# Kernel tuning notes

Hardware: AMD Instinct MI355X
Metric: run time of the kernel (lower is better)

The kernel has to match this reference:

```python
import jax, jax.numpy as jnp
from jax import lax
import numpy as np

K = 2        # k-hop MIS / number of rw SpGEMM iterations
EPS = 0.5    # lazy random-walk epsilon
N = 2048     # nodes
D = 512      # feature dim
E = 65536    # edges (avg degree 32)


def setup_inputs() -> dict:
    key = jax.random.key(0)
    k1, k2, k3, k4 = jax.random.split(key, 4)
    edge_index = jax.random.randint(k1, (2, E), 0, N, dtype=jnp.int32)
    edge_attr = jax.random.uniform(k2, (E,), dtype=jnp.float32)
    x = jax.random.normal(k3, (N, D), dtype=jnp.float32)
    rank = jnp.arange(N, dtype=jnp.int32)  # node ordering ('random' ordering = some permutation; identity here)
    u = jax.random.uniform(k4, (N, N), dtype=jnp.float32)  # noise for row-wise multinomial sampling
    return {"edge_index": edge_index, "edge_attr": edge_attr, "x": x, "rank": rank, "u": u}


def _maximal_k_independent_set(row, col, rank, n, k):
    """Greedy maximal k-independent set: nodes that are local rank-minima within k hops."""
    big = jnp.int32(n)

    def prop_min(r):  # one hop of min-propagation (message row -> col), keep self
        return jnp.minimum(jax.ops.segment_min(r[row], col, num_segments=n), r)

    def prop_or(b):   # one hop of boolean OR propagation (as int32)
        return jnp.maximum(jax.ops.segment_max(b[row], col, num_segments=n), b)

    def cond(st):
        mis, mask, mr = st
        return ~jnp.all(mask)

    def body(st):
        mis, mask, mr = st
        for _ in range(k):
            mr = prop_min(mr)
        mis = mis | (rank == mr)
        mk = mis.astype(jnp.int32)
        for _ in range(k):
            mk = prop_or(mk)
        mask = mk > 0
        mr = jnp.where(mask, big, rank)
        return mis, mask, mr

    init = (jnp.zeros(n, bool), jnp.zeros(n, bool), rank)
    mis, _, _ = lax.while_loop(cond, body, init)
    return mis


def _row_normalize(m):
    s = m.sum(axis=1, keepdims=True)
    return m / jnp.where(s > 0, s, 1.0)


def reference(edge_index, edge_attr, x, rank, u):
    n = x.shape[0]
    row, col = edge_index[0], edge_index[1]

    # --- MIS over the graph structure (integer-only) ---
    mis = _maximal_k_independent_set(row, col, rank, n, K)

    # --- adjacency (dense padded form of the SparseTensor) ---
    adj = jnp.zeros((n, n), x.dtype).at[row, col].add(edge_attr)

    # --- lazy random walk: rw = D^-1 A, offdiag *= (1-eps), diag = old_diag + eps ---
    rw = _row_normalize(adj)
    di = jnp.arange(n)
    new_diag = rw[di, di] + EPS  # computed BEFORE scaling, per original code
    rw = (rw * (1.0 - EPS)).at[di, di].set(new_diag)

    # --- c_mat = rw^K @ eye[:, mis]; padded to [n, n] with zero non-MIS columns ---
    c = jnp.where(mis[None, :], jnp.eye(n, dtype=x.dtype), 0.0)
    for _ in range(K):
        c = rw @ c
    c = _row_normalize(c)

    # --- sample_partition_matrix: per-row multinomial via Gumbel-argmax ---
    g = -jnp.log(-jnp.log(u + 1e-20) + 1e-20)
    logits = jnp.where(c > 0, jnp.log(jnp.maximum(c, 1e-30)), -jnp.inf) + g
    cluster = jnp.argmax(logits, axis=1)                 # [n] cluster id (a MIS column)
    c_hard = jax.nn.one_hot(cluster, n, dtype=x.dtype)   # partition matrix [n, n]

    # --- p_inv = row-normalized c_hard.T ---
    counts = c_hard.sum(axis=0)
    p_inv = c_hard.T / jnp.where(counts > 0, counts, 1.0)[:, None]

    # --- coarsen: c^T A c, pool: p_inv @ x ---
    adj_c = c_hard.T @ adj @ c_hard
    x_pool = p_inv @ x
    return adj_c, c_hard, p_inv, mis, x_pool
```

## Files before the change

kernel.cpp:

```cpp
#include <hip/hip_runtime.h>
#include <hip/hip_bf16.h>
#include <math.h>
#include <stdint.h>

#define NN 2048
#define DD 512
#define EE 65536
#define EPSV 0.5f
#define SEN 2048
#define PADE 98304

static const size_t SZ = (size_t)NN * NN;

__global__ __launch_bounds__(256) void count_deg(const int* __restrict__ row,
                                                 const int* __restrict__ col,
                                                 int* __restrict__ degree,
                                                 int* __restrict__ cdeg) {
  int e = blockIdx.x * 256 + threadIdx.x;
  atomicAdd(&degree[row[e]], 1);
  atomicAdd(&cdeg[col[e]], 1);
}

__global__ __launch_bounds__(1024) void csr_scan_pad(const int* __restrict__ degree,
                                                     const int* __restrict__ cdeg,
                                                     int* __restrict__ row_ptr,
                                                     int* __restrict__ fill_ptr,
                                                     int* __restrict__ col_ptr,
                                                     int* __restrict__ cfill_ptr,
                                                     unsigned short* __restrict__ colidx,
                                                     unsigned short* __restrict__ rowidx,
                                                     float* __restrict__ avals,
                                                     unsigned long long* __restrict__ packed,
                                                     int* __restrict__ counts) {
  __shared__ int a[NN], b[NN], c[NN], d[NN];
  int t = threadIdx.x;
  for (int v = t; v < NN; v += 1024) {
    a[v] = (degree[v] + 15) & ~15;
    c[v] = (cdeg[v] + 15) & ~15;
    packed[v] = 0ull;
    counts[v] = 0;
  }
  __syncthreads();
  int* s1 = a; int* d1 = b; int* s2 = c; int* d2 = d;
  for (int off = 1; off < NN; off <<= 1) {
    for (int v = t; v < NN; v += 1024) {
      d1[v] = s1[v] + (v >= off ? s1[v - off] : 0);
      d2[v] = s2[v] + (v >= off ? s2[v - off] : 0);
    }
    __syncthreads();
    int* tp = s1; s1 = d1; d1 = tp;
    tp = s2; s2 = d2; d2 = tp;
  }
  for (int v = t; v < NN; v += 1024) {
    int dg = degree[v];
    int end = s1[v];
    int excl = end - ((dg + 15) & ~15);
    row_ptr[v] = excl;
    fill_ptr[v] = excl;
    for (int e = excl + dg; e < end; ++e) {
      colidx[e] = (unsigned short)v;
      avals[e] = 0.f;
    }
    dg = cdeg[v];
    end = s2[v];
    excl = end - ((dg + 15) & ~15);
    col_ptr[v] = excl;
    cfill_ptr[v] = excl;
    for (int e = excl + dg; e < end; ++e) rowidx[e] = (unsigned short)v;
  }
  if (t == 0) {
    row_ptr[NN] = s1[NN - 1];
    col_ptr[NN] = s2[NN - 1];
  }
}

__global__ __launch_bounds__(256) void csr_fill(const int* __restrict__ row,
                                                const int* __restrict__ col,
                                                const float* __restrict__ attr,
                                                int* __restrict__ fill_ptr,
                                                int* __restrict__ cfill_ptr,
                                                unsigned short* __restrict__ colidx,
                                                unsigned short* __restrict__ rowidx,
                                                float* __restrict__ avals) {
  int e = blockIdx.x * 256 + threadIdx.x;
  int r = row[e], c = col[e];
  int pos = atomicAdd(&fill_ptr[r], 1);
  colidx[pos] = (unsigned short)c;
  avals[pos] = attr[e];
  rowidx[atomicAdd(&cfill_ptr[c], 1)] = (unsigned short)r;
}

__global__ __launch_bounds__(1024) void fused_mis_rw(const int* __restrict__ row_ptr_g,
                                                     const int* __restrict__ col_ptr_g,
                                                     const unsigned short* __restrict__ colidx,
                                                     const unsigned short* __restrict__ rowidx,
                                                     const int* __restrict__ rank_g,
                                                     int* __restrict__ mis_flag,
                                                     int* __restrict__ mis_list,
                                                     int* __restrict__ misinv,
                                                     int* __restrict__ mis_count,
                                                     const float* __restrict__ avals,
                                                     float* __restrict__ rw,
                                                     float* __restrict__ adjc,
                                                     float* __restrict__ xp) {
  if (blockIdx.x == 0) {
    __shared__ int rank_s[NN];
    __shared__ int mr[NN];
    __shared__ int cov[NN];
    __shared__ int dly[NN];
    __shared__ int mis_s[NN];
    __shared__ int row_ptr_s[NN + 1];
    __shared__ int col_ptr_s[NN + 1];
    __shared__ int unc[2][NN];
    __shared__ int dl[NN];
    __shared__ int ucnt[2];
    __shared__ int dcnt;
    __shared__ int cnt;
    int t = threadIdx.x;
    const uint4* col4 = (const uint4*)colidx;
    const uint4* row4 = (const uint4*)rowidx;

    for (int v = t; v < NN; v += 1024) {
      int rk = rank_g[v];
      rank_s[v] = rk;
      mr[v] = rk;
      cov[v] = 0;
      dly[v] = 0;
      mis_s[v] = 0;
      row_ptr_s[v] = row_ptr_g[v];
      col_ptr_s[v] = col_ptr_g[v];
      unc[0][v] = v;
    }
    if (t == 0) {
      row_ptr_s[NN] = row_ptr_g[NN];
      col_ptr_s[NN] = col_ptr_g[NN];
      ucnt[0] = NN;
      ucnt[1] = 0;
      dcnt = 0;
      cnt = 0;
    }
    __syncthreads();

    int cur = 0;
    for (int round = 0; round < NN; ++round) {
      int U = ucnt[cur];
      if (round) {
        for (int v = t; v < NN; v += 1024) {
          mr[v] = cov[v] ? SEN : rank_s[v];
          dly[v] = 0;
        }
        if (t == 0) { ucnt[cur ^ 1] = 0; dcnt = 0; }
        __syncthreads();
      }
      for (int i = t; i < U; i += 1024) {
        int v = unc[cur][i];
        int val = rank_s[v];
        int e0 = row_ptr_s[v];
        int nch = (row_ptr_s[v + 1] - e0) >> 3;
        const uint4* b4 = col4 + (e0 >> 3);
        for (int cI = 0; cI < nch; cI += 2) {
          uint4 A = b4[cI], B = b4[cI + 1];
          atomicMin(&mr[A.x & 0xFFFFu], val); atomicMin(&mr[A.x >> 16], val);
          atomicMin(&mr[A.y & 0xFFFFu], val); atomicMin(&mr[A.y >> 16], val);
          atomicMin(&mr[A.z & 0xFFFFu], val); atomicMin(&mr[A.z >> 16], val);
          atomicMin(&mr[A.w & 0xFFFFu], val); atomicMin(&mr[A.w >> 16], val);
          atomicMin(&mr[B.x & 0xFFFFu], val); atomicMin(&mr[B.x >> 16], val);
          atomicMin(&mr[B.y & 0xFFFFu], val); atomicMin(&mr[B.y >> 16], val);
          atomicMin(&mr[B.z & 0xFFFFu], val); atomicMin(&mr[B.z >> 16], val);
          atomicMin(&mr[B.w & 0xFFFFu], val); atomicMin(&mr[B.w >> 16], val);
        }
      }
      __syncthreads();
      for (int i = t; i < U; i += 1024) {
        int v = unc[cur][i];
        int val = mr[v];
        int e0 = col_ptr_s[v];
        int nch = (col_ptr_s[v + 1] - e0) >> 3;
        const uint4* b4 = row4 + (e0 >> 3);
        for (int cI = 0; cI < nch; cI += 2) {
          uint4 A = b4[cI], B = b4[cI + 1];
          int m0 = min(mr[A.x & 0xFFFFu], mr[A.x >> 16]);
          int m1 = min(mr[A.y & 0xFFFFu], mr[A.y >> 16]);
          int m2 = min(mr[A.z & 0xFFFFu], mr[A.z >> 16]);
          int m3 = min(mr[A.w & 0xFFFFu], mr[A.w >> 16]);
          int m4 = min(mr[B.x & 0xFFFFu], mr[B.x >> 16]);
          int m5 = min(mr[B.y & 0xFFFFu], mr[B.y >> 16]);
          int m6 = min(mr[B.z & 0xFFFFu], mr[B.z >> 16]);
          int m7 = min(mr[B.w & 0xFFFFu], mr[B.w >> 16]);
          val = min(val, min(min(min(m0, m1), min(m2, m3)),
                             min(min(m4, m5), min(m6, m7))));
        }
        if (rank_s[v] == val) {
          mis_s[v] = 1;
          dly[v] = 1;
          dl[atomicAdd(&dcnt, 1)] = v;
        }
      }
      __syncthreads();
      int D = dcnt;
      for (int i = t; i < D; i += 1024) {
        int v = dl[i];
        int e0 = row_ptr_s[v];
        int nch = (row_ptr_s[v + 1] - e0) >> 3;
        const uint4* b4 = col4 + (e0 >> 3);
        for (int cI = 0; cI < nch; cI += 2) {
          uint4 A = b4[cI], B = b4[cI + 1];
          dly[A.x & 0xFFFFu] = 1; dly[A.x >> 16] = 1;
          dly[A.y & 0xFFFFu] = 1; dly[A.y >> 16] = 1;
          dly[A.z & 0xFFFFu] = 1; dly[A.z >> 16] = 1;
          dly[A.w & 0xFFFFu] = 1; dly[A.w >> 16] = 1;
          dly[B.x & 0xFFFFu] = 1; dly[B.x >> 16] = 1;
          dly[B.y & 0xFFFFu] = 1; dly[B.y >> 16] = 1;
          dly[B.z & 0xFFFFu] = 1; dly[B.z >> 16] = 1;
          dly[B.w & 0xFFFFu] = 1; dly[B.w >> 16] = 1;
        }
      }
      __syncthreads();
      for (int i = t; i < U; i += 1024) {
        int v = unc[cur][i];
        int c1 = dly[v];
        if (!c1) {
          int e0 = col_ptr_s[v];
          int nch = (col_ptr_s[v + 1] - e0) >> 3;
          const uint4* b4 = row4 + (e0 >> 3);
          for (int cI = 0; cI < nch; cI += 2) {
            uint4 A = b4[cI], B = b4[cI + 1];
            c1 |= dly[A.x & 0xFFFFu] | dly[A.x >> 16] |
                  dly[A.y & 0xFFFFu] | dly[A.y >> 16] |
                  dly[A.z & 0xFFFFu] | dly[A.z >> 16] |
                  dly[A.w & 0xFFFFu] | dly[A.w >> 16] |
                  dly[B.x & 0xFFFFu] | dly[B.x >> 16] |
                  dly[B.y & 0xFFFFu] | dly[B.y >> 16] |
                  dly[B.z & 0xFFFFu] | dly[B.z >> 16] |
                  dly[B.w & 0xFFFFu] | dly[B.w >> 16];
            if (c1) break;
          }
        }
        if (c1) cov[v] = 1;
        else unc[cur ^ 1][atomicAdd(&ucnt[cur ^ 1], 1)] = v;
      }
      __syncthreads();
      if (ucnt[cur ^ 1] == 0) break;
      cur ^= 1;
    }

    for (int v = t; v < NN; v += 1024) {
      int s = mis_s[v];
      mis_flag[v] = s;
      int slot = -1;
      if (s) {
        slot = atomicAdd(&cnt, 1);
        mis_list[slot] = v;
      }
      misinv[v] = slot;
    }
    __syncthreads();
    if (t == 0) *mis_count = cnt;
  } else {
    __shared__ float rowbuf[NN];
    __shared__ float ssum;
    int i = blockIdx.x - 1;
    int t = threadIdx.x;
    float4 z4 = make_float4(0.f, 0.f, 0.f, 0.f);
    if (t < 512) ((float4*)(adjc + (size_t)i * NN))[t] = z4;
    if (t < 128) ((float4*)xp)[(size_t)i * 128 + t] = z4;
    for (int j = t; j < NN; j += 1024) rowbuf[j] = 0.f;
    if (t == 0) ssum = 0.f;
    __syncthreads();
    int e0 = row_ptr_g[i], e1 = row_ptr_g[i + 1];
    float part = 0.f;
    for (int e = e0 + t; e < e1; e += 1024) {
      float a = avals[e];
      atomicAdd(&rowbuf[colidx[e]], a);
      part += a;
    }
    for (int off = 32; off; off >>= 1) part += __shfl_down(part, off);
    if ((t & 63) == 0) atomicAdd(&ssum, part);
    __syncthreads();
    float s = ssum;
    s = (s > 0.f) ? s : 1.f;
    for (int j = t; j < NN; j += 1024) {
      float v = rowbuf[j] / s;
      v = (i == j) ? (v + EPSV) : (v * (1.f - EPSV));
      rw[(size_t)i * NN + j] = v;
    }
  }
}

__global__ __launch_bounds__(256) void bc_gather(const float* __restrict__ rw,
                                                 const int* __restrict__ mis_list,
                                                 const int* __restrict__ mis_count,
                                                 float* __restrict__ Bc) {
  int M = *mis_count;
  int total = M * NN;
  int stride = gridDim.x * 256;
  for (int j = blockIdx.x * 256 + threadIdx.x; j < total; j += stride) {
    int tc = j >> 11, i = j & (NN - 1);
    Bc[(size_t)tc * NN + i] = rw[(size_t)i * NN + mis_list[tc]];
  }
}

__device__ inline unsigned int f32_key(float x) {
  unsigned int u = __float_as_uint(x);
  return (u & 0x80000000u) ? ~u : (u | 0x80000000u);
}
__device__ inline float dot4(float4 a, float4 b) {
  return ((a.x * b.x + a.y * b.y) + (a.z * b.z + a.w * b.w));
}
__device__ inline unsigned long long umax64(unsigned long long a, unsigned long long b) {
  return a > b ? a : b;
}
__device__ inline int pdecode(unsigned long long p) {
  return (p == 0ull) ? 0 : (NN - 1 - (int)(p & 0xFFFFFFFFull));
}

__global__ __launch_bounds__(256) void c2_argmax(const float* __restrict__ rw,
                                                 const float* __restrict__ Bc,
                                                 const float* __restrict__ u,
                                                 const int* __restrict__ mis_list,
                                                 const int* __restrict__ mis_count,
                                                 unsigned long long* __restrict__ packed) {
  int M = *mis_count;
  int ncg = (M + 3) >> 2;
  int njobs = ncg * 64;
  int lane = threadIdx.x & 63, w = threadIdx.x >> 6;
  for (int j = blockIdx.x; j < njobs; j += gridDim.x) {
    int cg = j >> 6, tile = j & 63;
    int c0 = cg * 4;
    float4 creg[4][8];
    int mcol[4];
#pragma unroll
    for (int cc = 0; cc < 4; ++cc) {
      int colv = c0 + cc;
      int cl = colv < M ? colv : (M - 1);
      mcol[cc] = mis_list[cl];
      const float4* cb = (const float4*)(Bc + (size_t)cl * NN);
#pragma unroll
      for (int q = 0; q < 8; ++q) creg[cc][q] = cb[q * 64 + lane];
    }
    int rbase = tile * 32 + w * 8;
#pragma unroll
    for (int it = 0; it < 8; ++it) {
      int r = rbase + it;
      const float4* rp = (const float4*)(rw + (size_t)r * NN);
      float4 a0 = rp[lane], a1 = rp[64 + lane], a2 = rp[128 + lane], a3 = rp[192 + lane];
      float4 a4 = rp[256 + lane], a5 = rp[320 + lane], a6 = rp[384 + lane], a7 = rp[448 + lane];
      float sacc[4];
#pragma unroll
      for (int cc = 0; cc < 4; ++cc) {
        float s01 = dot4(a0, creg[cc][0]) + dot4(a1, creg[cc][1]);
        float s23 = dot4(a2, creg[cc][2]) + dot4(a3, creg[cc][3]);
        float s45 = dot4(a4, creg[cc][4]) + dot4(a5, creg[cc][5]);
        float s67 = dot4(a6, creg[cc][6]) + dot4(a7, creg[cc][7]);
        float s = (s01 + s23) + (s45 + s67);
        s += __shfl_xor(s, 32);
        s += __shfl_xor(s, 16);
        s += __shfl_xor(s, 8);
        s += __shfl_xor(s, 4);
        s += __shfl_xor(s, 2);
        s += __shfl_xor(s, 1);
        sacc[cc] = s;
      }
      if (lane == 0) {
        unsigned long long best = 0ull;
#pragma unroll
        for (int cc = 0; cc < 4; ++cc) {
          if (c0 + cc < M && sacc[cc] > 0.f) {
            int m = mcol[cc];
            float uu = u[(size_t)r * NN + m];
            float g = -logf(-logf(uu + 1e-20f) + 1e-20f);
            float logit = logf(sacc[cc]) + g;
            unsigned long long key =
                ((unsigned long long)f32_key(logit) << 32) | (unsigned int)(NN - 1 - m);
            best = umax64(best, key);
          }
        }
        if (best) atomicMax(&packed[r], best);
      }
    }
  }
}

__global__ __launch_bounds__(256) void decode_cnt(const unsigned long long* __restrict__ packed,
                                                  int* __restrict__ cluster,
                                                  int* __restrict__ counts) {
  int idx = blockIdx.x * 256 + threadIdx.x;
  int m = pdecode(packed[idx]);
  cluster[idx] = m;
  atomicAdd(&counts[m], 1);
}

__global__ __launch_bounds__(256) void scatter_chpm(const int* __restrict__ row,
                                                    const int* __restrict__ col,
                                                    const float* __restrict__ attr,
                                                    const float* __restrict__ x,
                                                    const int* __restrict__ cluster,
                                                    const int* __restrict__ counts,
                                                    const int* __restrict__ mis_flag,
                                                    float* __restrict__ out_ch,
                                                    float* __restrict__ out_pinv,
                                                    float* __restrict__ out_mis,
                                                    float* __restrict__ adjc,
                                                    float* __restrict__ xp) {
  int idx = blockIdx.x * 256 + threadIdx.x;
  int a = idx >> 11, b = idx & (NN - 1);
  out_ch[idx] = (cluster[a] == b) ? 1.f : 0.f;
  float pv = 0.f;
  if (cluster[b] == a) {
    int c = counts[a];
    pv = 1.f / (float)(c > 0 ? c : 1);
  }
  out_pinv[idx] = pv;
  if (idx < NN) out_mis[idx] = mis_flag[idx] ? 1.f : 0.f;
  if (idx < NN * DD) {
    int i = idx >> 9;
    int ci = cluster[i];
    int c = counts[ci];
    atomicAdd(&xp[ci * DD + (idx & (DD - 1))], x[idx] / (float)(c > 0 ? c : 1));
  }
  if (idx < EE) {
    atomicAdd(&adjc[(size_t)cluster[row[idx]] * NN + cluster[col[idx]]], attr[idx]);
  }
}

extern "C" void kernel_launch(void* const* d_in, const int* in_sizes, int n_in,
                              void* d_out, int out_size, void* d_ws, size_t ws_size,
                              hipStream_t stream) {
  const int*   edge_index = (const int*)d_in[0];
  const float* edge_attr  = (const float*)d_in[1];
  const float* x          = (const float*)d_in[2];
  const int*   rank       = (const int*)d_in[3];
  const float* u          = (const float*)d_in[4];
  float* out              = (float*)d_out;

  const int* row = edge_index;
  const int* col = edge_index + EE;

  float* out_adjc = out;
  float* out_ch   = out + SZ;
  float* out_pinv = out + 2 * SZ;
  float* out_mis  = out + 3 * SZ;
  float* out_xp   = out + 3 * SZ + NN;

  int*   degree    = (int*)d_ws;
  int*   cdeg      = degree + NN;
  unsigned long long* packed = (unsigned long long*)(cdeg + NN);
  int*   counts    = (int*)(packed + NN);
  int*   mis_flag  = counts + NN;
  int*   cluster   = mis_flag + NN;
  int*   mis_list  = cluster + NN;
  int*   misinv    = mis_list + NN;
  int*   mis_count = misinv + NN;
  int*   fill_ptr  = mis_count + 1;
  int*   cfill_ptr = fill_ptr + NN;
  int*   row_ptr   = cfill_ptr + NN;
  int*   col_ptr   = row_ptr + NN + 1;
  unsigned short* colidx =
      (unsigned short*)(((uintptr_t)(col_ptr + NN + 1) + 31) & ~(uintptr_t)31);
  unsigned short* rowidx = colidx + PADE;
  float* avals = (float*)(rowidx + PADE);

  hipMemsetAsync(d_ws, 0, 2 * NN * sizeof(int), stream);
  count_deg<<<EE / 256, 256, 0, stream>>>(row, col, degree, cdeg);
  csr_scan_pad<<<1, 1024, 0, stream>>>(degree, cdeg, row_ptr, fill_ptr, col_ptr,
                                       cfill_ptr, colidx, rowidx, avals, packed, counts);
  csr_fill<<<EE / 256, 256, 0, stream>>>(row, col, edge_attr, fill_ptr, cfill_ptr,
                                         colidx, rowidx, avals);
  fused_mis_rw<<<NN + 1, 1024, 0, stream>>>(row_ptr, col_ptr, colidx, rowidx, rank,
                                            mis_flag, mis_list, misinv, mis_count,
                                            avals, out_pinv , out_adjc, out_xp);
  bc_gather<<<256, 256, 0, stream>>>(out_pinv, mis_list, mis_count, out_ch);
  c2_argmax<<<1024, 256, 0, stream>>>(out_pinv, out_ch, u, mis_list, mis_count, packed);
  decode_cnt<<<NN / 256, 256, 0, stream>>>(packed, cluster, counts);
  scatter_chpm<<<(NN * NN) / 256, 256, 0, stream>>>(row, col, edge_attr, x, cluster,
                                                    counts, mis_flag, out_ch, out_pinv,
                                                    out_mis, out_adjc, out_xp);
}
```

Before: 234.6 us.

## Offload first MIS round to grid-wide kernels before single-block loop

Runs the first round of the k-hop MIS (two min-propagation hops, winner detection and two OR hops) in separate grid-wide kernels, with the first min hop fused into csr_fill through atomicMin. The single-block MIS loop inside fused_mis_rw then starts from the precomputed cover and MIS flags and only iterates over nodes still uncovered. This moves the heaviest, all-node round off the serial single-block critical path and onto many blocks. The cost is two extra kernel launches and extra global atomics in csr_fill. It also removes the unused misinv output.

```diff
diff --git a/kernel.cpp b/kernel.cpp
--- a/kernel.cpp
+++ b/kernel.cpp
@@ -23,6 +23,7 @@
 
 __global__ __launch_bounds__(1024) void csr_scan_pad(const int* __restrict__ degree,
                                                      const int* __restrict__ cdeg,
+                                                     const int* __restrict__ rank_g,
                                                      int* __restrict__ row_ptr,
                                                      int* __restrict__ fill_ptr,
                                                      int* __restrict__ col_ptr,
@@ -31,7 +32,9 @@
                                                      unsigned short* __restrict__ rowidx,
                                                      float* __restrict__ avals,
                                                      unsigned long long* __restrict__ packed,
-                                                     int* __restrict__ counts) {
+                                                     int* __restrict__ counts,
+                                                     int* __restrict__ mr1,
+                                                     int* __restrict__ covp) {
   __shared__ int a[NN], b[NN], c[NN], d[NN];
   int t = threadIdx.x;
   for (int v = t; v < NN; v += 1024) {
@@ -39,6 +42,8 @@
     c[v] = (cdeg[v] + 15) & ~15;
     packed[v] = 0ull;
     counts[v] = 0;
+    mr1[v] = rank_g[v];
+    covp[v] = 0;
   }
   __syncthreads();
   int* s1 = a; int* d1 = b; int* s2 = c; int* d2 = d;
@@ -77,17 +82,76 @@
 __global__ __launch_bounds__(256) void csr_fill(const int* __restrict__ row,
                                                 const int* __restrict__ col,
                                                 const float* __restrict__ attr,
+                                                const int* __restrict__ rank_g,
                                                 int* __restrict__ fill_ptr,
                                                 int* __restrict__ cfill_ptr,
                                                 unsigned short* __restrict__ colidx,
                                                 unsigned short* __restrict__ rowidx,
-                                                float* __restrict__ avals) {
+                                                float* __restrict__ avals,
+                                                int* __restrict__ mr1) {
   int e = blockIdx.x * 256 + threadIdx.x;
   int r = row[e], c = col[e];
   int pos = atomicAdd(&fill_ptr[r], 1);
   colidx[pos] = (unsigned short)c;
   avals[pos] = attr[e];
   rowidx[atomicAdd(&cfill_ptr[c], 1)] = (unsigned short)r;
+  atomicMin(&mr1[c], rank_g[r]);
+}
+
+__global__ __launch_bounds__(256) void min2_detect(const int* __restrict__ row_ptr,
+                                                   const int* __restrict__ col_ptr,
+                                                   const unsigned short* __restrict__ colidx,
+                                                   const unsigned short* __restrict__ rowidx,
+                                                   const int* __restrict__ rank_g,
+                                                   const int* __restrict__ mr1,
+                                                   int* __restrict__ mis0,
+                                                   int* __restrict__ covp) {
+  int v = blockIdx.x * 256 + threadIdx.x;
+  int val = mr1[v];
+  int e0 = col_ptr[v], e1 = col_ptr[v + 1];
+  const uint4* r4 = (const uint4*)rowidx;
+  for (int cI = e0 >> 3; cI < (e1 >> 3); ++cI) {
+    uint4 A = r4[cI];
+    int m0 = min(mr1[A.x & 0xFFFFu], mr1[A.x >> 16]);
+    int m1 = min(mr1[A.y & 0xFFFFu], mr1[A.y >> 16]);
+    int m2 = min(mr1[A.z & 0xFFFFu], mr1[A.z >> 16]);
+    int m3 = min(mr1[A.w & 0xFFFFu], mr1[A.w >> 16]);
+    val = min(val, min(min(m0, m1), min(m2, m3)));
+  }
+  int isw = (rank_g[v] == val) ? 1 : 0;
+  mis0[v] = isw;
+  if (isw) {
+    covp[v] = 1;
+    int f0 = row_ptr[v], f1 = row_ptr[v + 1];
+    const uint4* c4 = (const uint4*)colidx;
+    for (int cI = f0 >> 3; cI < (f1 >> 3); ++cI) {
+      uint4 A = c4[cI];
+      covp[A.x & 0xFFFFu] = 1; covp[A.x >> 16] = 1;
+      covp[A.y & 0xFFFFu] = 1; covp[A.y >> 16] = 1;
+      covp[A.z & 0xFFFFu] = 1; covp[A.z >> 16] = 1;
+      covp[A.w & 0xFFFFu] = 1; covp[A.w >> 16] = 1;
+    }
+  }
+}
+
+__global__ __launch_bounds__(256) void or_hop(const int* __restrict__ col_ptr,
+                                              const unsigned short* __restrict__ rowidx,
+                                              const int* __restrict__ covp,
+                                              int* __restrict__ cov2) {
+  int v = blockIdx.x * 256 + threadIdx.x;
+  int b = covp[v];
+  if (!b) {
+    int e0 = col_ptr[v], e1 = col_ptr[v + 1];
+    const uint4* r4 = (const uint4*)rowidx;
+    for (int cI = e0 >> 3; cI < (e1 >> 3) && !b; ++cI) {
+      uint4 A = r4[cI];
+      b = covp[A.x & 0xFFFFu] | covp[A.x >> 16] |
+          covp[A.y & 0xFFFFu] | covp[A.y >> 16] |
+          covp[A.z & 0xFFFFu] | covp[A.z >> 16] |
+          covp[A.w & 0xFFFFu] | covp[A.w >> 16];
+    }
+  }
+  cov2[v] = b ? 1 : 0;
 }
 
 __global__ __launch_bounds__(1024) void fused_mis_rw(const int* __restrict__ row_ptr_g,
@@ -95,9 +159,10 @@
                                                      const unsigned short* __restrict__ colidx,
                                                      const unsigned short* __restrict__ rowidx,
                                                      const int* __restrict__ rank_g,
+                                                     const int* __restrict__ mis0_g,
+                                                     const int* __restrict__ cov2_g,
                                                      int* __restrict__ mis_flag,
                                                      int* __restrict__ mis_list,
-                                                     int* __restrict__ misinv,
                                                      int* __restrict__ mis_count,
                                                      const float* __restrict__ avals,
                                                      float* __restrict__ rw,
@@ -121,138 +186,132 @@
     const uint4* row4 = (const uint4*)rowidx;
 
     for (int v = t; v < NN; v += 1024) {
-      int rk = rank_g[v];
-      rank_s[v] = rk;
-      mr[v] = rk;
-      cov[v] = 0;
-      dly[v] = 0;
-      mis_s[v] = 0;
+      rank_s[v] = rank_g[v];
+      cov[v] = cov2_g[v];
+      mis_s[v] = mis0_g[v];
       row_ptr_s[v] = row_ptr_g[v];
       col_ptr_s[v] = col_ptr_g[v];
-      unc[0][v] = v;
     }
     if (t == 0) {
       row_ptr_s[NN] = row_ptr_g[NN];
       col_ptr_s[NN] = col_ptr_g[NN];
-      ucnt[0] = NN;
+      ucnt[0] = 0;
       ucnt[1] = 0;
       dcnt = 0;
       cnt = 0;
     }
     __syncthreads();
+    for (int v = t; v < NN; v += 1024)
+      if (!cov[v]) unc[0][atomicAdd(&ucnt[0], 1)] = v;
+    __syncthreads();
 
     int cur = 0;
-    for (int round = 0; round < NN; ++round) {
-      int U = ucnt[cur];
-      if (round) {
+    if (ucnt[0] > 0) {
+      for (int round = 0; round < NN; ++round) {
+        int U = ucnt[cur];
         for (int v = t; v < NN; v += 1024) {
           mr[v] = cov[v] ? SEN : rank_s[v];
           dly[v] = 0;
         }
         if (t == 0) { ucnt[cur ^ 1] = 0; dcnt = 0; }
         __syncthreads();
-      }
-      for (int i = t; i < U; i += 1024) {
-        int v = unc[cur][i];
-        int val = rank_s[v];
-        int e0 = row_ptr_s[v];
-        int nch = (row_ptr_s[v + 1] - e0) >> 3;
-        const uint4* b4 = col4 + (e0 >> 3);
-        for (int cI = 0; cI < nch; cI += 2) {
-          uint4 A = b4[cI], B = b4[cI + 1];
-          atomicMin(&mr[A.x & 0xFFFFu], val); atomicMin(&mr[A.x >> 16], val);
-          atomicMin(&mr[A.y & 0xFFFFu], val); atomicMin(&mr[A.y >> 16], val);
-          atomicMin(&mr[A.z & 0xFFFFu], val); atomicMin(&mr[A.z >> 16], val);
-          atomicMin(&mr[A.w & 0xFFFFu], val); atomicMin(&mr[A.w >> 16], val);
-          atomicMin(&mr[B.x & 0xFFFFu], val); atomicMin(&mr[B.x >> 16], val);
-          atomicMin(&mr[B.y & 0xFFFFu], val); atomicMin(&mr[B.y >> 16], val);
-          atomicMin(&mr[B.z & 0xFFFFu], val); atomicMin(&mr[B.z >> 16], val);
-          atomicMin(&mr[B.w & 0xFFFFu], val); atomicMin(&mr[B.w >> 16], val);
+        for (int i = t; i < U; i += 1024) {
+          int v = unc[cur][i];
+          int val = rank_s[v];
+          int e0 = row_ptr_s[v];
+          int nch = (row_ptr_s[v + 1] - e0) >> 3;
+          const uint4* b4 = col4 + (e0 >> 3);
+          for (int cI = 0; cI < nch; cI += 2) {
+            uint4 A = b4[cI], B = b4[cI + 1];
+            atomicMin(&mr[A.x & 0xFFFFu], val); atomicMin(&mr[A.x >> 16], val);
+            atomicMin(&mr[A.y & 0xFFFFu], val); atomicMin(&mr[A.y >> 16], val);
+            atomicMin(&mr[A.z & 0xFFFFu], val); atomicMin(&mr[A.z >> 16], val);
+            atomicMin(&mr[A.w & 0xFFFFu], val); atomicMin(&mr[A.w >> 16], val);
+            atomicMin(&mr[B.x & 0xFFFFu], val); atomicMin(&mr[B.x >> 16], val);
+            atomicMin(&mr[B.y & 0xFFFFu], val); atomicMin(&mr[B.y >> 16], val);
+            atomicMin(&mr[B.z & 0xFFFFu], val); atomicMin(&mr[B.z >> 16], val);
+            atomicMin(&mr[B.w & 0xFFFFu], val); atomicMin(&mr[B.w >> 16], val);
+          }
         }
-      }
-      __syncthreads();
-      for (int i = t; i < U; i += 1024) {
-        int v = unc[cur][i];
-        int val = mr[v];
-        int e0 = col_ptr_s[v];
-        int nch = (col_ptr_s[v + 1] - e0) >> 3;
-        const uint4* b4 = row4 + (e0 >> 3);
-        for (int cI = 0; cI < nch; cI += 2) {
-          uint4 A = b4[cI], B = b4[cI + 1];
-          int m0 = min(mr[A.x & 0xFFFFu], mr[A.x >> 16]);
-          int m1 = min(mr[A.y & 0xFFFFu], mr[A.y >> 16]);
-          int m2 = min(mr[A.z & 0xFFFFu], mr[A.z >> 16]);
-          int m3 = min(mr[A.w & 0xFFFFu], mr[A.w >> 16]);
-          int m4 = min(mr[B.x & 0xFFFFu], mr[B.x >> 16]);
-          int m5 = min(mr[B.y & 0xFFFFu], mr[B.y >> 16]);
-          int m6 = min(mr[B.z & 0xFFFFu], mr[B.z >> 16]);
-          int m7 = min(mr[B.w & 0xFFFFu], mr[B.w >> 16]);
-          val = min(val, min(min(min(m0, m1), min(m2, m3)),
-                             min(min(m4, m5), min(m6, m7))));
-        }
-        if (rank_s[v] == val) {
-          mis_s[v] = 1;
-          dly[v] = 1;
-          dl[atomicAdd(&dcnt, 1)] = v;
-        }
-      }
-      __syncthreads();
-      int D = dcnt;
-      for (int i = t; i < D; i += 1024) {
-        int v = dl[i];
-        int e0 = row_ptr_s[v];
-        int nch = (row_ptr_s[v + 1] - e0) >> 3;
-        const uint4* b4 = col4 + (e0 >> 3);
-        for (int cI = 0; cI < nch; cI += 2) {
-          uint4 A = b4[cI], B = b4[cI + 1];
-          dly[A.x & 0xFFFFu] = 1; dly[A.x >> 16] = 1;
-          dly[A.y & 0xFFFFu] = 1; dly[A.y >> 16] = 1;
-          dly[A.z & 0xFFFFu] = 1; dly[A.z >> 16] = 1;
-          dly[A.w & 0xFFFFu] = 1; dly[A.w >> 16] = 1;
-          dly[B.x & 0xFFFFu] = 1; dly[B.x >> 16] = 1;
-          dly[B.y & 0xFFFFu] = 1; dly[B.y >> 16] = 1;
-          dly[B.z & 0xFFFFu] = 1; dly[B.z >> 16] = 1;
-          dly[B.w & 0xFFFFu] = 1; dly[B.w >> 16] = 1;
-        }
-      }
-      __syncthreads();
-      for (int i = t; i < U; i += 1024) {
-        int v = unc[cur][i];
-        int c1 = dly[v];
-        if (!c1) {
+        __syncthreads();
+        for (int i = t; i < U; i += 1024) {
+          int v = unc[cur][i];
+          int val = mr[v];
           int e0 = col_ptr_s[v];
           int nch = (col_ptr_s[v + 1] - e0) >> 3;
           const uint4* b4 = row4 + (e0 >> 3);
           for (int cI = 0; cI < nch; cI += 2) {
             uint4 A = b4[cI], B = b4[cI + 1];
-            c1 |= dly[A.x & 0xFFFFu] | dly[A.x >> 16] |
-                  dly[A.y & 0xFFFFu] | dly[A.y >> 16] |
-                  dly[A.z & 0xFFFFu] | dly[A.z >> 16] |
-                  dly[A.w & 0xFFFFu] | dly[A.w >> 16] |
-                  dly[B.x & 0xFFFFu] | dly[B.x >> 16] |
-                  dly[B.y & 0xFFFFu] | dly[B.y >> 16] |
-                  dly[B.z & 0xFFFFu] | dly[B.z >> 16] |
-                  dly[B.w & 0xFFFFu] | dly[B.w >> 16];
-            if (c1) break;
+            int m0 = min(mr[A.x & 0xFFFFu], mr[A.x >> 16]);
+            int m1 = min(mr[A.y & 0xFFFFu], mr[A.y >> 16]);
+            int m2 = min(mr[A.z & 0xFFFFu], mr[A.z >> 16]);
+            int m3 = min(mr[A.w & 0xFFFFu], mr[A.w >> 16]);
+            int m4 = min(mr[B.x & 0xFFFFu], mr[B.x >> 16]);
+            int m5 = min(mr[B.y & 0xFFFFu], mr[B.y >> 16]);
+            int m6 = min(mr[B.z & 0xFFFFu], mr[B.z >> 16]);
+            int m7 = min(mr[B.w & 0xFFFFu], mr[B.w >> 16]);
+            val = min(val, min(min(min(m0, m1), min(m2, m3)),
+                               min(min(m4, m5), min(m6, m7))));
+          }
+          if (rank_s[v] == val) {
+            mis_s[v] = 1;
+            dly[v] = 1;
+            dl[atomicAdd(&dcnt, 1)] = v;
           }
         }
-        if (c1) cov[v] = 1;
-        else unc[cur ^ 1][atomicAdd(&ucnt[cur ^ 1], 1)] = v;
+        __syncthreads();
+        int D = dcnt;
+        for (int i = t; i < D; i += 1024) {
+          int v = dl[i];
+          int e0 = row_ptr_s[v];
+          int nch = (row_ptr_s[v + 1] - e0) >> 3;
+          const uint4* b4 = col4 + (e0 >> 3);
+          for (int cI = 0; cI < nch; cI += 2) {
+            uint4 A = b4[cI], B = b4[cI + 1];
+            dly[A.x & 0xFFFFu] = 1; dly[A.x >> 16] = 1;
+            dly[A.y & 0xFFFFu] = 1; dly[A.y >> 16] = 1;
+            dly[A.z & 0xFFFFu] = 1; dly[A.z >> 16] = 1;
+            dly[A.w & 0xFFFFu] = 1; dly[A.w >> 16] = 1;
+            dly[B.x & 0xFFFFu] = 1; dly[B.x >> 16] = 1;
+            dly[B.y & 0xFFFFu] = 1; dly[B.y >> 16] = 1;
+            dly[B.z & 0xFFFFu] = 1; dly[B.z >> 16] = 1;
+            dly[B.w & 0xFFFFu] = 1; dly[B.w >> 16] = 1;
+          }
+        }
+        __syncthreads();
+        for (int i = t; i < U; i += 1024) {
+          int v = unc[cur][i];
+          int c1 = dly[v];
+          if (!c1) {
+            int e0 = col_ptr_s[v];
+            int nch = (col_ptr_s[v + 1] - e0) >> 3;
+            const uint4* b4 = row4 + (e0 >> 3);
+            for (int cI = 0; cI < nch; cI += 2) {
+              uint4 A = b4[cI], B = b4[cI + 1];
+              c1 |= dly[A.x & 0xFFFFu] | dly[A.x >> 16] |
+                    dly[A.y & 0xFFFFu] | dly[A.y >> 16] |
+                    dly[A.z & 0xFFFFu] | dly[A.z >> 16] |
+                    dly[A.w & 0xFFFFu] | dly[A.w >> 16] |
+                    dly[B.x & 0xFFFFu] | dly[B.x >> 16] |
+                    dly[B.y & 0xFFFFu] | dly[B.y >> 16] |
+                    dly[B.z & 0xFFFFu] | dly[B.z >> 16] |
+                    dly[B.w & 0xFFFFu] | dly[B.w >> 16];
+              if (c1) break;
+            }
+          }
+          if (c1) cov[v] = 1;
+          else unc[cur ^ 1][atomicAdd(&ucnt[cur ^ 1], 1)] = v;
+        }
+        __syncthreads();
+        if (ucnt[cur ^ 1] == 0) break;
+        cur ^= 1;
       }
-      __syncthreads();
-      if (ucnt[cur ^ 1] == 0) break;
-      cur ^= 1;
     }
 
     for (int v = t; v < NN; v += 1024) {
       int s = mis_s[v];
       mis_flag[v] = s;
-      int slot = -1;
-      if (s) {
-        slot = atomicAdd(&cnt, 1);
-        mis_list[slot] = v;
-      }
-      misinv[v] = slot;
+      if (s) mis_list[atomicAdd(&cnt, 1)] = v;
     }
     __syncthreads();
     if (t == 0) *mis_count = cnt;
@@ -449,25 +508,32 @@
   int*   mis_flag  = counts + NN;
   int*   cluster   = mis_flag + NN;
   int*   mis_list  = cluster + NN;
-  int*   misinv    = mis_list + NN;
-  int*   mis_count = misinv + NN;
+  int*   mis_count = mis_list + NN;
   int*   fill_ptr  = mis_count + 1;
   int*   cfill_ptr = fill_ptr + NN;
   int*   row_ptr   = cfill_ptr + NN;
   int*   col_ptr   = row_ptr + NN + 1;
+  int*   mr1       = col_ptr + NN + 1;
+  int*   mis0      = mr1 + NN;
+  int*   covp      = mis0 + NN;
+  int*   cov2      = covp + NN;
   unsigned short* colidx =
-      (unsigned short*)(((uintptr_t)(col_ptr + NN + 1) + 31) & ~(uintptr_t)31);
+      (unsigned short*)(((uintptr_t)(cov2 + NN) + 31) & ~(uintptr_t)31);
   unsigned short* rowidx = colidx + PADE;
   float* avals = (float*)(rowidx + PADE);
 
   hipMemsetAsync(d_ws, 0, 2 * NN * sizeof(int), stream);
   count_deg<<<EE / 256, 256, 0, stream>>>(row, col, degree, cdeg);
-  csr_scan_pad<<<1, 1024, 0, stream>>>(degree, cdeg, row_ptr, fill_ptr, col_ptr,
-                                       cfill_ptr, colidx, rowidx, avals, packed, counts);
-  csr_fill<<<EE / 256, 256, 0, stream>>>(row, col, edge_attr, fill_ptr, cfill_ptr,
-                                         colidx, rowidx, avals);
+  csr_scan_pad<<<1, 1024, 0, stream>>>(degree, cdeg, rank, row_ptr, fill_ptr, col_ptr,
+                                       cfill_ptr, colidx, rowidx, avals, packed, counts,
+                                       mr1, covp);
+  csr_fill<<<EE / 256, 256, 0, stream>>>(row, col, edge_attr, rank, fill_ptr, cfill_ptr,
+                                         colidx, rowidx, avals, mr1);
+  min2_detect<<<NN / 256, 256, 0, stream>>>(row_ptr, col_ptr, colidx, rowidx, rank,
+                                            mr1, mis0, covp);
+  or_hop<<<NN / 256, 256, 0, stream>>>(col_ptr, rowidx, covp, cov2);
   fused_mis_rw<<<NN + 1, 1024, 0, stream>>>(row_ptr, col_ptr, colidx, rowidx, rank,
-                                            mis_flag, mis_list, misinv, mis_count,
+                                            mis0, cov2, mis_flag, mis_list, mis_count,
                                             avals, out_pinv , out_adjc, out_xp);
   bc_gather<<<256, 256, 0, stream>>>(out_pinv, mis_list, mis_count, out_ch);
   c2_argmax<<<1024, 256, 0, stream>>>(out_pinv, out_ch, u, mis_list, mis_count, packed);
```

Measured after the change: 240.4 us. 2.5% more time.

## Fuse column gather, GEMV argmax and decode into one row-owned kernel

Applied to the files above, without the earlier changes.

Three kernels (column gather into a B buffer, c2 dot-product argmax with global atomicMax, decode/count) become one kernel. Each wave keeps two rw rows in registers and loops over all MIS columns, which it gathers per block into shared-memory tiles of 8 columns. The best key is reduced per row in registers, so the packed array, its atomics and two launches go away. The trade-off is that every one of the 256 blocks re-gathers all MIS columns with strided global reads, and only 256 blocks of 4 waves with 64KB LDS each may limit occupancy.

```diff
diff --git a/kernel.cpp b/kernel.cpp
--- a/kernel.cpp
+++ b/kernel.cpp
@@ -9,6 +9,7 @@
 #define EPSV 0.5f
 #define SEN 2048
 #define PADE 98304
+#define CTILE 8
 
 static const size_t SZ = (size_t)NN * NN;
 
@@ -30,14 +31,12 @@
                                                      unsigned short* __restrict__ colidx,
                                                      unsigned short* __restrict__ rowidx,
                                                      float* __restrict__ avals,
-                                                     unsigned long long* __restrict__ packed,
                                                      int* __restrict__ counts) {
   __shared__ int a[NN], b[NN], c[NN], d[NN];
   int t = threadIdx.x;
   for (int v = t; v < NN; v += 1024) {
     a[v] = (degree[v] + 15) & ~15;
     c[v] = (cdeg[v] + 15) & ~15;
-    packed[v] = 0ull;
     counts[v] = 0;
   }
   __syncthreads();
@@ -287,19 +286,6 @@
   }
 }
 
-__global__ __launch_bounds__(256) void bc_gather(const float* __restrict__ rw,
-                                                 const int* __restrict__ mis_list,
-                                                 const int* __restrict__ mis_count,
-                                                 float* __restrict__ Bc) {
-  int M = *mis_count;
-  int total = M * NN;
-  int stride = gridDim.x * 256;
-  for (int j = blockIdx.x * 256 + threadIdx.x; j < total; j += stride) {
-    int tc = j >> 11, i = j & (NN - 1);
-    Bc[(size_t)tc * NN + i] = rw[(size_t)i * NN + mis_list[tc]];
-  }
-}
-
 __device__ inline unsigned int f32_key(float x) {
   unsigned int u = __float_as_uint(x);
   return (u & 0x80000000u) ? ~u : (u | 0x80000000u);
@@ -314,80 +300,88 @@
   return (p == 0ull) ? 0 : (NN - 1 - (int)(p & 0xFFFFFFFFull));
 }
 
-__global__ __launch_bounds__(256) void c2_argmax(const float* __restrict__ rw,
-                                                 const float* __restrict__ Bc,
-                                                 const float* __restrict__ u,
-                                                 const int* __restrict__ mis_list,
-                                                 const int* __restrict__ mis_count,
-                                                 unsigned long long* __restrict__ packed) {
-  int M = *mis_count;
-  int ncg = (M + 3) >> 2;
-  int njobs = ncg * 64;
-  int lane = threadIdx.x & 63, w = threadIdx.x >> 6;
-  for (int j = blockIdx.x; j < njobs; j += gridDim.x) {
-    int cg = j >> 6, tile = j & 63;
-    int c0 = cg * 4;
-    float4 creg[4][8];
-    int mcol[4];
-#pragma unroll
-    for (int cc = 0; cc < 4; ++cc) {
-      int colv = c0 + cc;
-      int cl = colv < M ? colv : (M - 1);
-      mcol[cc] = mis_list[cl];
-      const float4* cb = (const float4*)(Bc + (size_t)cl * NN);
-#pragma unroll
-      for (int q = 0; q < 8; ++q) creg[cc][q] = cb[q * 64 + lane];
-    }
-    int rbase = tile * 32 + w * 8;
-#pragma unroll
-    for (int it = 0; it < 8; ++it) {
-      int r = rbase + it;
-      const float4* rp = (const float4*)(rw + (size_t)r * NN);
-      float4 a0 = rp[lane], a1 = rp[64 + lane], a2 = rp[128 + lane], a3 = rp[192 + lane];
-      float4 a4 = rp[256 + lane], a5 = rp[320 + lane], a6 = rp[384 + lane], a7 = rp[448 + lane];
-      float sacc[4];
-#pragma unroll
-      for (int cc = 0; cc < 4; ++cc) {
-        float s01 = dot4(a0, creg[cc][0]) + dot4(a1, creg[cc][1]);
-        float s23 = dot4(a2, creg[cc][2]) + dot4(a3, creg[cc][3]);
-        float s45 = dot4(a4, creg[cc][4]) + dot4(a5, creg[cc][5]);
-        float s67 = dot4(a6, creg[cc][6]) + dot4(a7, creg[cc][7]);
-        float s = (s01 + s23) + (s45 + s67);
-        s += __shfl_xor(s, 32);
-        s += __shfl_xor(s, 16);
-        s += __shfl_xor(s, 8);
-        s += __shfl_xor(s, 4);
-        s += __shfl_xor(s, 2);
-        s += __shfl_xor(s, 1);
-        sacc[cc] = s;
-      }
-      if (lane == 0) {
-        unsigned long long best = 0ull;
-#pragma unroll
-        for (int cc = 0; cc < 4; ++cc) {
-          if (c0 + cc < M && sacc[cc] > 0.f) {
-            int m = mcol[cc];
-            float uu = u[(size_t)r * NN + m];
-            float g = -logf(-logf(uu + 1e-20f) + 1e-20f);
-            float logit = logf(sacc[cc]) + g;
-            unsigned long long key =
-                ((unsigned long long)f32_key(logit) << 32) | (unsigned int)(NN - 1 - m);
-            best = umax64(best, key);
-          }
-        }
-        if (best) atomicMax(&packed[r], best);
-      }
-    }
-  }
-}
-
-__global__ __launch_bounds__(256) void decode_cnt(const unsigned long long* __restrict__ packed,
+__global__ __launch_bounds__(256) void c2_cluster(const float* __restrict__ rw,
+                                                  const float* __restrict__ u,
+                                                  const int* __restrict__ mis_list,
+                                                  const int* __restrict__ mis_count,
                                                   int* __restrict__ cluster,
                                                   int* __restrict__ counts) {
-  int idx = blockIdx.x * 256 + threadIdx.x;
-  int m = pdecode(packed[idx]);
-  cluster[idx] = m;
-  atomicAdd(&counts[m], 1);
+  __shared__ float Bs[CTILE][NN];
+  int M = *mis_count;
+  int t = threadIdx.x;
+  int lane = t & 63, w = t >> 6;
+  int r0 = blockIdx.x * 8 + w * 2;
+  const float4* rp0 = (const float4*)(rw + (size_t)r0 * NN);
+  const float4* rp1 = (const float4*)(rw + (size_t)(r0 + 1) * NN);
+  float4 A0[8], A1[8];
+#pragma unroll
+  for (int q = 0; q < 8; ++q) {
+    A0[q] = rp0[q * 64 + lane];
+    A1[q] = rp1[q * 64 + lane];
+  }
+  unsigned long long best0 = 0ull, best1 = 0ull;
+  for (int c0 = 0; c0 < M; c0 += CTILE) {
+    int c1 = min(CTILE, M - c0);
+    __syncthreads();
+    for (int idx = t; idx < c1 * NN; idx += 256) {
+      int c = idx >> 11, i = idx & (NN - 1);
+      Bs[c][i] = rw[(size_t)i * NN + mis_list[c0 + c]];
+    }
+    __syncthreads();
+    for (int jj = 0; jj < c1; ++jj) {
+      int m = mis_list[c0 + jj];
+      const float4* bb = (const float4*)(Bs[jj]);
+      float4 B[8];
+#pragma unroll
+      for (int q = 0; q < 8; ++q) B[q] = bb[q * 64 + lane];
+      float s01 = dot4(A0[0], B[0]) + dot4(A0[1], B[1]);
+      float s23 = dot4(A0[2], B[2]) + dot4(A0[3], B[3]);
+      float s45 = dot4(A0[4], B[4]) + dot4(A0[5], B[5]);
+      float s67 = dot4(A0[6], B[6]) + dot4(A0[7], B[7]);
+      float s = (s01 + s23) + (s45 + s67);
+      s += __shfl_xor(s, 32);
+      s += __shfl_xor(s, 16);
+      s += __shfl_xor(s, 8);
+      s += __shfl_xor(s, 4);
+      s += __shfl_xor(s, 2);
+      s += __shfl_xor(s, 1);
+      float t01 = dot4(A1[0], B[0]) + dot4(A1[1], B[1]);
+      float t23 = dot4(A1[2], B[2]) + dot4(A1[3], B[3]);
+      float t45 = dot4(A1[4], B[4]) + dot4(A1[5], B[5]);
+      float t67 = dot4(A1[6], B[6]) + dot4(A1[7], B[7]);
+      float tt = (t01 + t23) + (t45 + t67);
+      tt += __shfl_xor(tt, 32);
+      tt += __shfl_xor(tt, 16);
+      tt += __shfl_xor(tt, 8);
+      tt += __shfl_xor(tt, 4);
+      tt += __shfl_xor(tt, 2);
+      tt += __shfl_xor(tt, 1);
+      if (lane == 0) {
+        if (s > 0.f) {
+          float uu = u[(size_t)r0 * NN + m];
+          float g = -logf(-logf(uu + 1e-20f) + 1e-20f);
+          float logit = logf(s) + g;
+          best0 = umax64(best0, ((unsigned long long)f32_key(logit) << 32) |
+                                    (unsigned int)(NN - 1 - m));
+        }
+        if (tt > 0.f) {
+          float uu = u[(size_t)(r0 + 1) * NN + m];
+          float g = -logf(-logf(uu + 1e-20f) + 1e-20f);
+          float logit = logf(tt) + g;
+          best1 = umax64(best1, ((unsigned long long)f32_key(logit) << 32) |
+                                    (unsigned int)(NN - 1 - m));
+        }
+      }
+    }
+  }
+  if (lane == 0) {
+    int m0b = pdecode(best0);
+    cluster[r0] = m0b;
+    atomicAdd(&counts[m0b], 1);
+    int m1b = pdecode(best1);
+    cluster[r0 + 1] = m1b;
+    atomicAdd(&counts[m1b], 1);
+  }
 }
 
 __global__ __launch_bounds__(256) void scatter_chpm(const int* __restrict__ row,
@@ -444,8 +438,7 @@
 
   int*   degree    = (int*)d_ws;
   int*   cdeg      = degree + NN;
-  unsigned long long* packed = (unsigned long long*)(cdeg + NN);
-  int*   counts    = (int*)(packed + NN);
+  int*   counts    = cdeg + NN;
   int*   mis_flag  = counts + NN;
   int*   cluster   = mis_flag + NN;
   int*   mis_list  = cluster + NN;
@@ -463,15 +456,13 @@
   hipMemsetAsync(d_ws, 0, 2 * NN * sizeof(int), stream);
   count_deg<<<EE / 256, 256, 0, stream>>>(row, col, degree, cdeg);
   csr_scan_pad<<<1, 1024, 0, stream>>>(degree, cdeg, row_ptr, fill_ptr, col_ptr,
-                                       cfill_ptr, colidx, rowidx, avals, packed, counts);
+                                       cfill_ptr, colidx, rowidx, avals, counts);
   csr_fill<<<EE / 256, 256, 0, stream>>>(row, col, edge_attr, fill_ptr, cfill_ptr,
                                          colidx, rowidx, avals);
   fused_mis_rw<<<NN + 1, 1024, 0, stream>>>(row_ptr, col_ptr, colidx, rowidx, rank,
                                             mis_flag, mis_list, misinv, mis_count,
                                             avals, out_pinv , out_adjc, out_xp);
-  bc_gather<<<256, 256, 0, stream>>>(out_pinv, mis_list, mis_count, out_ch);
-  c2_argmax<<<1024, 256, 0, stream>>>(out_pinv, out_ch, u, mis_list, mis_count, packed);
-  decode_cnt<<<NN / 256, 256, 0, stream>>>(packed, cluster, counts);
+  c2_cluster<<<256, 256, 0, stream>>>(out_pinv, u, mis_list, mis_count, cluster, counts);
   scatter_chpm<<<(NN * NN) / 256, 256, 0, stream>>>(row, col, edge_attr, x, cluster,
                                                     counts, mis_flag, out_ch, out_pinv,
                                                     out_mis, out_adjc, out_xp);
```

Measured after the change: 262.9 us. 12.1% more time.
